# Kernel tuning notes

Measured on AMD Instinct MI355X. Metric: run time of the kernel, lower is better.

The kernel has to match this reference:

```python
import jax, jax.numpy as jnp
import numpy as np

T, N, E = 4, 20000, 320000
F_IN, EH, NH, GH, OUT = 12, 32, 64, 64, 1
NUM_LAYERS = 2
EB_IN = (EH + 2 * NH) * 2 + GH  # 384
NB_IN = 2 * NH + 2 * EH + GH    # 256
GB_IN = NH + EH + GH            # 160


def setup_inputs() -> dict:
    key = jax.random.key(0)
    ks = jax.random.split(key, 24)
    f32 = jnp.float32
    def w(k, fan_in, shape):
        return jax.random.normal(k, shape, f32) * (1.0 / np.sqrt(fan_in))
    return {
        "node_attr": jax.random.normal(ks[0], (T, N, F_IN), f32),
        "edge_attr": jax.random.normal(ks[1], (T, E, 1), f32),
        "edge_index": jax.random.randint(ks[2], (2, E), 0, N, jnp.int32),
        "sp_L_vals": jax.random.normal(ks[3], (E,), f32),
        "global_attr": jax.random.normal(ks[4], (1, GH), f32),
        "coeff": jnp.full((1,), 0.1, f32),
        "W_ee": w(ks[5], 1, (1, EH)), "b_ee": jnp.zeros((EH,), f32),
        "W_ne": w(ks[6], F_IN, (F_IN, NH)), "b_ne": jnp.zeros((NH,), f32),
        "W_eb": w(ks[7], EB_IN, (EB_IN, EH)), "b_eb": jnp.zeros((EH,), f32),
        "W_nb": w(ks[8], NB_IN, (NB_IN, NH)), "b_nb": jnp.zeros((NH,), f32),
        "W_gb": w(ks[9], GB_IN, (GB_IN, GH)), "b_gb": jnp.zeros((GH,), f32),
        "W_nd1": w(ks[10], NH, (NH, NH)), "b_nd1": jnp.zeros((NH,), f32),
        "W_nd2": w(ks[11], NH, (NH, OUT)), "b_nd2": jnp.zeros((OUT,), f32),
    }


def _forward(node_attr, edge_attr, edge_index, sp_L_vals, global_attr, coeff,
             W_ee, b_ee, W_ne, b_ne, W_eb, b_eb, W_nb, b_nb, W_gb, b_gb,
             W_nd1, b_nd1, W_nd2, b_nd2):
    relu = jax.nn.relu
    s, r = edge_index[0], edge_index[1]
    seg = lambda v, idx: jax.ops.segment_sum(v, idx, num_segments=N)
    c = coeff[0]

    # encoders
    x_enc = relu(node_attr @ W_ne + b_ne)   # [T,N,NH]
    e_enc = relu(edge_attr @ W_ee + b_ee)   # [T,E,EH]

    def run_gn(xT, eT, g0):
        # recurrent GN core over processing steps; hidden (h_x,h_e,h_g) starts at zeros
        def step(carry, inp):
            h_x, h_e, h_g = carry
            x_in, e_in = inp
            gE = jnp.broadcast_to(h_g, (E, GH))
            # EdgeBlock: [edge_in, edge_h, sender_in, sender_h, recv_in, recv_h, global]
            edge_cat = jnp.concatenate(
                [e_in, h_e, x_in[s], h_x[s], x_in[r], h_x[r], gE], axis=-1)
            e_new = relu(edge_cat @ W_eb + b_eb)              # [E,EH]
            sent = seg(e_new, s)                              # scatter_add by sender
            recv = seg(e_new, r)                              # scatter_add by receiver
            gN = jnp.broadcast_to(h_g, (N, GH))
            node_cat = jnp.concatenate([x_in, h_x, sent, recv, gN], axis=-1)
            x_new = relu(node_cat @ W_nb + b_nb)              # [N,NH]
            # GlobalBlock: scatter_mean == plain mean (single graph)
            g_cat = jnp.concatenate(
                [x_new.mean(0, keepdims=True), e_new.mean(0, keepdims=True), h_g], axis=-1)
            g_new = relu(g_cat @ W_gb + b_gb)                 # [1,GH]
            # physics terms (pde='diff'): time derivative = state update,
            # spatial derivative = coeff * (graph-Laplacian action via sp_L edge weights)
            t_der = x_new - h_x
            s_der = c * seg(sp_L_vals[:, None] * (x_new[s] - x_new[r]), r)
            return (x_new, e_new, g_new), (x_new, e_new, g_new, t_der, s_der)
        carry0 = (jnp.zeros((N, NH), jnp.float32), jnp.zeros((E, EH), jnp.float32), g0)
        _, ys = jax.lax.scan(step, carry0, (xT, eT))
        return ys  # xs[T,N,NH], es[T,E,EH], gs[T,1,GH], td[T,N,NH], sd[T,N,NH]

    xs, es, gs, td, sd = run_gn(x_enc, e_enc, global_attr)
    x_pre = x_enc
    for _ in range(NUM_LAYERS - 1):
        x_res = xs + x_pre          # residual node state feeds next GN layer
        x_pre = x_res
        xs, es, gs, td, sd = run_gn(x_res, es, gs[0])

    x_final = xs + x_pre            # add_residual=True final residual
    h = relu(x_final @ W_nd1 + b_nd1)
    out_nodes = h @ W_nd2 + b_nd2   # [T,N,OUT]
    return out_nodes, td, sd


def reference(node_attr, edge_attr, edge_index, sp_L_vals, global_attr, coeff,
              W_ee, b_ee, W_ne, b_ne, W_eb, b_eb, W_nb, b_nb, W_gb, b_gb,
              W_nd1, b_nd1, W_nd2, b_nd2):
    return _forward(node_attr, edge_attr, edge_index, sp_L_vals, global_attr, coeff,
                    W_ee, b_ee, W_ne, b_ne, W_eb, b_eb, W_nb, b_nb, W_gb, b_gb,
                    W_nd1, b_nd1, W_nd2, b_nd2)
```

## Files before the change

kernel.cpp:

```cpp
#include <hip/hip_runtime.h>


typedef __attribute__((ext_vector_type(8))) short s16x8;
typedef __attribute__((ext_vector_type(4))) float f32x4;

#define T_STEPS 4
#define NN 20000
#define NP 20224
#define NE 320000

__device__ __forceinline__ float bf2f(unsigned short h){
  return __uint_as_float(((unsigned)h)<<16);
}
__device__ __forceinline__ unsigned short f2bf(float f){
  unsigned u = __float_as_uint(f);
  return (unsigned short)((u + 0x7fffu + ((u>>16)&1u)) >> 16);
}
__device__ __forceinline__ float loadIn(const void* p, size_t i, int bf){
  return bf ? bf2f(((const unsigned short*)p)[i]) : ((const float*)p)[i];
}
__device__ __forceinline__ void storeOut(void* o, size_t i, float v, int bf){
  if(bf) ((unsigned short*)o)[i] = f2bf(v);
  else   ((float*)o)[i] = v;
}
__device__ __forceinline__ void load8(const float* __restrict__ p, float* v){
  const float4* q4 = (const float4*)p;
  float4 a = q4[0], b = q4[1];
  v[0]=a.x; v[1]=a.y; v[2]=a.z; v[3]=a.w;
  v[4]=b.x; v[5]=b.y; v[6]=b.z; v[7]=b.w;
}
__device__ __forceinline__ int4 pack8(const float* v){
  unsigned p0 = (unsigned)f2bf(v[0]) | ((unsigned)f2bf(v[1])<<16);
  unsigned p1 = (unsigned)f2bf(v[2]) | ((unsigned)f2bf(v[3])<<16);
  unsigned p2 = (unsigned)f2bf(v[4]) | ((unsigned)f2bf(v[5])<<16);
  unsigned p3 = (unsigned)f2bf(v[6]) | ((unsigned)f2bf(v[7])<<16);
  return make_int4((int)p0,(int)p1,(int)p2,(int)p3);
}
__device__ __forceinline__ void unp8(int4 w, float* a){
  unsigned x;
  x=(unsigned)w.x; a[0]=__uint_as_float(x<<16); a[1]=__uint_as_float(x&0xffff0000u);
  x=(unsigned)w.y; a[2]=__uint_as_float(x<<16); a[3]=__uint_as_float(x&0xffff0000u);
  x=(unsigned)w.z; a[4]=__uint_as_float(x<<16); a[5]=__uint_as_float(x&0xffff0000u);
  x=(unsigned)w.w; a[6]=__uint_as_float(x<<16); a[7]=__uint_as_float(x&0xffff0000u);
}

union I4S8 { int4 i; s16x8 s; };

__global__ void probe_kernel(const void* coeff_in, int* flagp, float* coeff_f){
  unsigned short u = ((const unsigned short*)coeff_in)[0];
  float as_bf = bf2f(u);
  int f = (fabsf(as_bf - 0.1f) < 0.02f) ? 1 : 0;
  *flagp = f;
  *coeff_f = f ? as_bf : ((const float*)coeff_in)[0];
}

struct ConvJob { const void* src; float* dst; int n; };
struct ConvJobs { ConvJob j[16]; int cnt; };

__global__ void conv_kernel(ConvJobs jobs, const int* flagp, float* z, int zn){
  int bf = *flagp;
  int tid = blockIdx.x*blockDim.x + threadIdx.x;
  int stride = gridDim.x*blockDim.x;
  for(int q=0;q<jobs.cnt;q++){
    const void* s = jobs.j[q].src; float* d = jobs.j[q].dst; int n = jobs.j[q].n;
    for(int i=tid;i<n;i+=stride) d[i] = loadIn(s, i, bf);
  }
  for(int i=tid;i<zn;i+=stride) z[i]=0.f;
}

__global__ void csr_hist(const int* __restrict__ ei, int* deg_s, int* deg_r,
                         unsigned short* __restrict__ rank_s,
                         unsigned short* __restrict__ rank_r){
  int e = blockIdx.x*256+threadIdx.x;
  rank_s[e] = (unsigned short)atomicAdd(&deg_s[ei[e]],1);
  rank_r[e] = (unsigned short)atomicAdd(&deg_r[ei[NE+e]],1);
}

__global__ void csr_scan(const int* __restrict__ deg_s, int* __restrict__ off_s,
                         const int* __restrict__ deg_r, int* __restrict__ off_r){
  const int CH = NP/256;
  const int* deg = blockIdx.x ? deg_r : deg_s;
  int* off = blockIdx.x ? off_r : off_s;
  int t = threadIdx.x;
  int base = t*CH;
  int s = 0;
  #pragma unroll 8
  for(int i=0;i<CH;i++) s += deg[base+i];
  int lane = t & 63, w = t >> 6;
  int x = s;
  #pragma unroll
  for(int o=1;o<64;o<<=1){
    int y = __shfl_up(x, o, 64);
    if(lane >= o) x += y;
  }
  __shared__ int wtot[4];
  if(lane==63) wtot[w] = x;
  __syncthreads();
  int wbase = 0;
  #pragma unroll
  for(int k=0;k<3;k++) if(k<w) wbase += wtot[k];
  int acc = wbase + x - s;
  #pragma unroll 8
  for(int i=0;i<CH;i++){
    off[base+i]=acc; acc+=deg[base+i];
  }
  if(t==255) off[NN]=acc;
}

__global__ void csr_fill(const int* __restrict__ ei,
                         const int* __restrict__ s_off, const int* __restrict__ r_off,
                         const unsigned short* __restrict__ rank_s,
                         const unsigned short* __restrict__ rank_r,
                         int* __restrict__ csr_s, int* __restrict__ csr_r,
                         int2* __restrict__ sr2){
  int e = blockIdx.x*256+threadIdx.x;
  int s = ei[e], r = ei[NE+e];
  sr2[e] = make_int2(s,r);
  csr_s[s_off[s]+rank_s[e]] = e;
  csr_r[r_off[r]+rank_r[e]] = e;
}

__global__ void pack_w_kernel(const void* __restrict__ W,
                              unsigned short* __restrict__ P, int KW, int NT,
                              const int* flagp){
  int bf = *flagp;
  int idx = blockIdx.x*blockDim.x + threadIdx.x;
  int total = NT*KW*512;
  if(idx>=total) return;
  int j = idx & 7;
  int lane = (idx>>3) & 63;
  int rest = idx >> 9;
  int kw = rest % KW;
  int nt = rest / KW;
  int k = kw*32 + (lane>>4)*8 + j;
  int n = nt*16 + (lane&15);
  P[idx] = f2bf(loadIn(W, (size_t)k*(NT*16) + n, bf));
}

__global__ void node_enc_kernel(const void* __restrict__ na,
                                const float* __restrict__ W, const float* __restrict__ b,
                                unsigned short* __restrict__ xA, const int* flagp){
  __shared__ float arow[4][12];
  int bf = *flagp;
  int lane = threadIdx.x & 63, nl = threadIdx.x >> 6;
  int row = blockIdx.x*4 + nl;
  if(lane<12) arow[nl][lane] = loadIn(na, (size_t)row*12+lane, bf);
  __syncthreads();
  float acc = b[lane];
  #pragma unroll
  for(int k=0;k<12;k++) acc += arow[nl][k]*W[k*64+lane];
  xA[(size_t)row*64+lane] = f2bf(fmaxf(acc,0.f));
}

__global__ __launch_bounds__(256) void edge_block_mfma(
  const int2* __restrict__ sr2,
  const unsigned short* __restrict__ x_in,
  const unsigned short* __restrict__ h_x,
  const void* __restrict__ e_attr,
  int e_attr_off,
  const unsigned short* __restrict__ e_in,
  const unsigned short* __restrict__ h_e,
  const float* __restrict__ g,
  const float* __restrict__ W_ee, const float* __restrict__ b_ee,
  const unsigned short* __restrict__ Wp,
  const float* __restrict__ b_eb,
  unsigned short* __restrict__ e_out,
  float* __restrict__ partial_e,
  const int* flagp)
{
  const int tid = threadIdx.x;
  const int lane = tid&63;
  const int q = lane>>4, m16 = lane&15;
  const int pair = blockIdx.x*4 + (tid>>6);
  const int e0 = pair*32;
  const int eg0 = e0 + m16, eg1 = e0 + 16 + m16;
  const int2 sr0 = sr2[eg0], sr1 = sr2[eg1];
  const int o8 = q*8;
  const int4 z4 = make_int4(0,0,0,0);

  I4S8 A0[12], A1[12];
  if(e_attr){
    int bf = *flagp;
    float a0v = loadIn(e_attr, (size_t)e_attr_off + eg0, bf);
    float a1v = loadIn(e_attr, (size_t)e_attr_off + eg1, bf);
    float v[8];
    #pragma unroll
    for(int j=0;j<8;j++) v[j] = fmaxf(a0v*W_ee[o8+j]+b_ee[o8+j], 0.f);
    A0[0].i = pack8(v);
    #pragma unroll
    for(int j=0;j<8;j++) v[j] = fmaxf(a1v*W_ee[o8+j]+b_ee[o8+j], 0.f);
    A1[0].i = pack8(v);
  } else {
    A0[0].i = ((const int4*)(e_in + (size_t)eg0*32))[q];
    A1[0].i = ((const int4*)(e_in + (size_t)eg1*32))[q];
  }
  A0[1].i = h_e ? ((const int4*)(h_e + (size_t)eg0*32))[q] : z4;
  A1[1].i = h_e ? ((const int4*)(h_e + (size_t)eg1*32))[q] : z4;
  { const int4* p0 = (const int4*)(x_in + (size_t)sr0.x*64);
    const int4* p1 = (const int4*)(x_in + (size_t)sr1.x*64);
    A0[2].i = p0[q]; A1[2].i = p1[q];
    A0[3].i = p0[4+q]; A1[3].i = p1[4+q]; }
  if(h_x){
    const int4* p0 = (const int4*)(h_x + (size_t)sr0.x*64);
    const int4* p1 = (const int4*)(h_x + (size_t)sr1.x*64);
    A0[4].i = p0[q]; A1[4].i = p1[q];
    A0[5].i = p0[4+q]; A1[5].i = p1[4+q];
  } else { A0[4].i=z4; A1[4].i=z4; A0[5].i=z4; A1[5].i=z4; }
  { const int4* p0 = (const int4*)(x_in + (size_t)sr0.y*64);
    const int4* p1 = (const int4*)(x_in + (size_t)sr1.y*64);
    A0[6].i = p0[q]; A1[6].i = p1[q];
    A0[7].i = p0[4+q]; A1[7].i = p1[4+q]; }
  if(h_x){
    const int4* p0 = (const int4*)(h_x + (size_t)sr0.y*64);
    const int4* p1 = (const int4*)(h_x + (size_t)sr1.y*64);
    A0[8].i = p0[q]; A1[8].i = p1[q];
    A0[9].i = p0[4+q]; A1[9].i = p1[4+q];
  } else { A0[8].i=z4; A1[8].i=z4; A0[9].i=z4; A1[9].i=z4; }
  { float v[8];
    load8(g + o8, v);      A0[10].i = pack8(v); A1[10].i = A0[10].i;
    load8(g + 32 + o8, v); A0[11].i = pack8(v); A1[11].i = A0[11].i; }

  f32x4 a00={0.f,0.f,0.f,0.f}, a01={0.f,0.f,0.f,0.f};
  f32x4 a10={0.f,0.f,0.f,0.f}, a11={0.f,0.f,0.f,0.f};
  #pragma unroll
  for(int kw=0;kw<12;kw++){
    s16x8 b0 = *(const s16x8*)(Wp + (size_t)(kw*64 + lane)*8);
    s16x8 b1 = *(const s16x8*)(Wp + (size_t)((12+kw)*64 + lane)*8);
    a00 = __builtin_amdgcn_mfma_f32_16x16x32_bf16(A0[kw].s, b0, a00, 0,0,0);
    a01 = __builtin_amdgcn_mfma_f32_16x16x32_bf16(A0[kw].s, b1, a01, 0,0,0);
    a10 = __builtin_amdgcn_mfma_f32_16x16x32_bf16(A1[kw].s, b0, a10, 0,0,0);
    a11 = __builtin_amdgcn_mfma_f32_16x16x32_bf16(A1[kw].s, b1, a11, 0,0,0);
  }

  float pe0=0.f, pe1=0.f;
  const float bb0 = b_eb[m16], bb1 = b_eb[16+m16];
  #pragma unroll
  for(int r=0;r<4;r++){
    int eg0m = e0 + q*4 + r;
    int eg1m = eg0m + 16;
    float v00 = fmaxf(a00[r]+bb0, 0.f);
    float v01 = fmaxf(a01[r]+bb1, 0.f);
    float v10 = fmaxf(a10[r]+bb0, 0.f);
    float v11 = fmaxf(a11[r]+bb1, 0.f);
    e_out[(size_t)eg0m*32+m16]    = f2bf(v00);
    e_out[(size_t)eg0m*32+16+m16] = f2bf(v01);
    e_out[(size_t)eg1m*32+m16]    = f2bf(v10);
    e_out[(size_t)eg1m*32+16+m16] = f2bf(v11);
    pe0 += v00+v10; pe1 += v01+v11;
  }
  pe0 += __shfl_xor(pe0,16,64); pe0 += __shfl_xor(pe0,32,64);
  pe1 += __shfl_xor(pe1,16,64); pe1 += __shfl_xor(pe1,32,64);
  if(q==0){
    int slot = blockIdx.x & 63;
    atomicAdd(&partial_e[slot*32+m16],    pe0);
    atomicAdd(&partial_e[slot*32+16+m16], pe1);
  }
}

__global__ void aggregate_kernel(const unsigned short* __restrict__ e_new,
  const int* __restrict__ s_off, const int* __restrict__ csr_s,
  const int* __restrict__ r_off, const int* __restrict__ csr_r,
  unsigned short* __restrict__ sentB, unsigned short* __restrict__ recvB)
{
  int node = blockIdx.x*4 + (threadIdx.x>>6);
  int lane = threadIdx.x & 63;
  int f = lane & 31, j = lane >> 5;
  float aS0=0.f, aS1=0.f, aR0=0.f, aR1=0.f;
  {
    int beg = s_off[node], end = s_off[node+1];
    int i = beg + j;
    for(; i+2<end; i+=4){
      aS0 += bf2f(e_new[(size_t)csr_s[i]*32 + f]);
      aS1 += bf2f(e_new[(size_t)csr_s[i+2]*32 + f]);
    }
    for(; i<end; i+=2)
      aS0 += bf2f(e_new[(size_t)csr_s[i]*32 + f]);
  }
  {
    int beg = r_off[node], end = r_off[node+1];
    int i = beg + j;
    for(; i+2<end; i+=4){
      aR0 += bf2f(e_new[(size_t)csr_r[i]*32 + f]);
      aR1 += bf2f(e_new[(size_t)csr_r[i+2]*32 + f]);
    }
    for(; i<end; i+=2)
      aR0 += bf2f(e_new[(size_t)csr_r[i]*32 + f]);
  }
  float accS = aS0+aS1, accR = aR0+aR1;
  accS += __shfl_xor(accS,32,64);
  accR += __shfl_xor(accR,32,64);
  if(j==0){
    sentB[(size_t)node*32+f] = f2bf(accS);
    recvB[(size_t)node*32+f] = f2bf(accR);
  }
}

__global__ __launch_bounds__(256) void node_block_mfma(
  const unsigned short* __restrict__ x_in, const unsigned short* __restrict__ h_x,
  const unsigned short* __restrict__ sentB, const unsigned short* __restrict__ recvB,
  const float* __restrict__ g,
  const unsigned short* __restrict__ Wp,
  const float* __restrict__ b_nb,
  unsigned short* __restrict__ x_out, float* __restrict__ partial_x,
  void* __restrict__ out_base, size_t td_off, int has_td,
  const int* flagp)
{
  const int tid = threadIdx.x, lane = tid&63;
  const int q = lane>>4, m16 = lane&15;
  const int tile = blockIdx.x*4 + (tid>>6);
  if(tile >= NN/16) return;
  const int n0 = tile*16;
  const int ng = n0+m16;
  const int o8 = q*8;
  const int4 z4 = make_int4(0,0,0,0);

  I4S8 A[8];
  { const int4* xp = (const int4*)(x_in + (size_t)ng*64);
    A[0].i = xp[q]; A[1].i = xp[4+q]; }
  if(h_x){ const int4* hp = (const int4*)(h_x + (size_t)ng*64);
    A[2].i = hp[q]; A[3].i = hp[4+q];
  } else { A[2].i = z4; A[3].i = z4; }
  A[4].i = ((const int4*)(sentB + (size_t)ng*32))[q];
  A[5].i = ((const int4*)(recvB + (size_t)ng*32))[q];
  { float v[8];
    load8(g + o8, v);      A[6].i = pack8(v);
    load8(g + 32 + o8, v); A[7].i = pack8(v); }

  f32x4 acc[4];
  #pragma unroll
  for(int nt=0;nt<4;nt++) acc[nt] = (f32x4){0.f,0.f,0.f,0.f};
  #pragma unroll
  for(int kw=0;kw<8;kw++){
    #pragma unroll
    for(int nt=0;nt<4;nt++){
      s16x8 b = *(const s16x8*)(Wp + (size_t)((nt*8+kw)*64 + lane)*8);
      acc[nt] = __builtin_amdgcn_mfma_f32_16x16x32_bf16(A[kw].s, b, acc[nt], 0,0,0);
    }
  }

  int bf = has_td ? *flagp : 0;
  float ps[4] = {0.f,0.f,0.f,0.f};
  #pragma unroll
  for(int r=0;r<4;r++){
    int nodeg = n0 + q*4 + r;
    #pragma unroll
    for(int nt=0;nt<4;nt++){
      int col = nt*16 + m16;
      float vv = fmaxf(acc[nt][r] + b_nb[col], 0.f);
      x_out[(size_t)nodeg*64+col] = f2bf(vv);
      if(has_td){
        float hxv = h_x ? bf2f(h_x[(size_t)nodeg*64+col]) : 0.f;
        storeOut(out_base, td_off + (size_t)nodeg*64+col, vv - hxv, bf);
      }
      ps[nt] += vv;
    }
  }
  #pragma unroll
  for(int nt=0;nt<4;nt++){
    ps[nt] += __shfl_xor(ps[nt],16,64);
    ps[nt] += __shfl_xor(ps[nt],32,64);
  }
  if(q==0){
    int slot = blockIdx.x & 63;
    #pragma unroll
    for(int nt=0;nt<4;nt++)
      atomicAdd(&partial_x[slot*64 + nt*16 + m16], ps[nt]);
  }
}

__global__ void global_block_kernel(float* __restrict__ partial_x,
  float* __restrict__ partial_e, const float* __restrict__ h_g,
  const float* __restrict__ W_gb, const float* __restrict__ b_gb,
  float* __restrict__ g_out)
{
  __shared__ float gcat[160];
  __shared__ float red[4][64];
  int tid = threadIdx.x;
  if(tid<64){
    float sx = 0.f;
    #pragma unroll 8
    for(int i=0;i<64;i++) sx += partial_x[i*64+tid];
    gcat[tid] = sx * (1.0f/(float)NN);
  } else if(tid<96){
    int j = tid-64;
    float se = 0.f;
    #pragma unroll 8
    for(int i=0;i<64;i++) se += partial_e[i*32+j];
    gcat[64+j] = se * (1.0f/(float)NE);
  } else if(tid<160){
    gcat[tid] = h_g[tid-96];
  }
  __syncthreads();
  int j = tid&63, c = tid>>6;
  float acc = 0.f;
  #pragma unroll 8
  for(int k=c*40;k<c*40+40;k++) acc += gcat[k]*W_gb[k*64+j];
  red[c][j] = acc;
  __syncthreads();
  for(int i=tid;i<2048;i+=256) partial_e[i]=0.f;
  for(int i=tid;i<4096;i+=256) partial_x[i]=0.f;
  if(tid<64){
    float a = red[0][tid]+red[1][tid]+red[2][tid]+red[3][tid] + b_gb[tid];
    g_out[tid] = fmaxf(a, 0.f);
  }
}

__global__ void sder_csr_kernel(const int2* __restrict__ sr2,
  const void* __restrict__ spL, const unsigned short* __restrict__ x_new,
  const int* __restrict__ r_off, const int* __restrict__ csr_r,
  const float* __restrict__ coeff, void* __restrict__ out_base, size_t off,
  const int* flagp)
{
  int bf = *flagp;
  int lane = threadIdx.x&63, nl = threadIdx.x>>6;
  int node = blockIdx.x*4+nl;
  float xn = bf2f(x_new[(size_t)node*64+lane]);
  float a0=0.f, a1=0.f, a2=0.f, a3=0.f;
  int beg = r_off[node], end = r_off[node+1];
  int i = beg;
  for(; i+4<=end; i+=4){
    int e1 = csr_r[i], e2 = csr_r[i+1], e3 = csr_r[i+2], e4 = csr_r[i+3];
    float w1 = loadIn(spL, e1, bf), w2 = loadIn(spL, e2, bf);
    float w3 = loadIn(spL, e3, bf), w4 = loadIn(spL, e4, bf);
    int s1 = sr2[e1].x, s2 = sr2[e2].x, s3 = sr2[e3].x, s4 = sr2[e4].x;
    a0 += w1*(bf2f(x_new[(size_t)s1*64+lane])-xn);
    a1 += w2*(bf2f(x_new[(size_t)s2*64+lane])-xn);
    a2 += w3*(bf2f(x_new[(size_t)s3*64+lane])-xn);
    a3 += w4*(bf2f(x_new[(size_t)s4*64+lane])-xn);
  }
  for(; i<end; i++){
    int e1 = csr_r[i];
    float w1 = loadIn(spL, e1, bf);
    a0 += w1*(bf2f(x_new[(size_t)sr2[e1].x*64+lane])-xn);
  }
  storeOut(out_base, off + (size_t)node*64+lane, coeff[0]*((a0+a1)+(a2+a3)), bf);
}

__global__ void add_bf16_kernel(const unsigned short* __restrict__ a,
  const unsigned short* __restrict__ b, unsigned short* __restrict__ c, int n){
  int i = blockIdx.x*blockDim.x+threadIdx.x;
  int stride = gridDim.x*blockDim.x;
  for(;i<n;i+=stride) c[i] = f2bf(bf2f(a[i])+bf2f(b[i]));
}

__global__ __launch_bounds__(256) void decoder_kernel(
  const unsigned short* __restrict__ xs, const unsigned short* __restrict__ xr,
  const unsigned short* __restrict__ WpD,
  const float* __restrict__ b1, const float* __restrict__ W2,
  const float* __restrict__ b2,
  void* __restrict__ out_base, const int* flagp)
{
  const int tid=threadIdx.x, lane=tid&63;
  const int q=lane>>4, m16=lane&15;
  const int tile = blockIdx.x*4 + (tid>>6);
  const int row0 = tile*16;
  const int rg = row0 + m16;

  I4S8 A[2];
  #pragma unroll
  for(int kw=0;kw<2;kw++){
    int4 xa = ((const int4*)(xs + (size_t)rg*64 + kw*32))[q];
    int4 xb = ((const int4*)(xr + (size_t)rg*64 + kw*32))[q];
    float va[8], vb[8], v[8];
    unp8(xa, va); unp8(xb, vb);
    #pragma unroll
    for(int j=0;j<8;j++) v[j] = va[j]+vb[j];
    A[kw].i = pack8(v);
  }

  f32x4 acc[4];
  #pragma unroll
  for(int nt=0;nt<4;nt++) acc[nt] = (f32x4){0.f,0.f,0.f,0.f};
  #pragma unroll
  for(int kw=0;kw<2;kw++){
    #pragma unroll
    for(int nt=0;nt<4;nt++){
      s16x8 b = *(const s16x8*)(WpD + (size_t)((nt*2+kw)*64 + lane)*8);
      acc[nt] = __builtin_amdgcn_mfma_f32_16x16x32_bf16(A[kw].s, b, acc[nt], 0,0,0);
    }
  }

  float val[4];
  #pragma unroll
  for(int r=0;r<4;r++){
    float s = 0.f;
    #pragma unroll
    for(int nt=0;nt<4;nt++){
      int col = nt*16 + m16;
      s += fmaxf(acc[nt][r] + b1[col], 0.f) * W2[col];
    }
    val[r] = s;
  }
  #pragma unroll
  for(int o=1;o<16;o<<=1){
    #pragma unroll
    for(int r=0;r<4;r++) val[r] += __shfl_xor(val[r], o, 64);
  }
  if(m16==0){
    int bf = *flagp;
    float bb = b2[0];
    #pragma unroll
    for(int r=0;r<4;r++)
      storeOut(out_base, (size_t)(row0 + q*4 + r), val[r] + bb, bf);
  }
}

extern "C" void kernel_launch(void* const* d_in, const int* in_sizes, int n_in,
                              void* d_out, int out_size, void* d_ws, size_t ws_size,
                              hipStream_t stream){
  const void* node_attr = d_in[0];
  const void* edge_attr = d_in[1];
  const int*  ei        = (const int*)d_in[2];
  const void* spL       = d_in[3];
  const void* gattr     = d_in[4];
  const void* coeff_in  = d_in[5];
  const void* W_ee_in = d_in[6];  const void* b_ee_in = d_in[7];
  const void* W_ne_in = d_in[8];  const void* b_ne_in = d_in[9];
  const void* W_eb_in = d_in[10]; const void* b_eb_in = d_in[11];
  const void* W_nb_in = d_in[12]; const void* b_nb_in = d_in[13];
  const void* W_gb_in = d_in[14]; const void* b_gb_in = d_in[15];
  const void* W_nd1_in= d_in[16]; const void* b_nd1_in= d_in[17];
  const void* W_nd2_in= d_in[18]; const void* b_nd2_in= d_in[19];

  float* ws = (float*)d_ws;
  float* W_ee_f = ws;             float* b_ee_f = W_ee_f+32;
  float* W_ne_f = b_ee_f+32;      float* b_ne_f = W_ne_f+768;
  float* W_gb_f = b_ne_f+64;      float* b_gb_f = W_gb_f+10240;
  float* W_nd1_f= b_gb_f+64;      float* b_nd1_f= W_nd1_f+4096;
  float* W_nd2_f= b_nd1_f+64;     float* b_nd2_f= W_nd2_f+64;
  float* b_eb_f = b_nd2_f+1;      float* b_nb_f = b_eb_f+32;
  float* coeff_f= b_nb_f+64;
  int*   flagp  = (int*)(ws + 15523);
  float* gbuf   = ws + 15524;
  float* part_e = ws + 16100;
  float* part_x = part_e + 2048;
  int*   deg_s  = (int*)(part_x + 4096);
  int*   deg_r  = deg_s + NP;
  int*   s_off  = deg_r + NP;
  int*   r_off  = s_off + NP+1;
  unsigned short* rank_s = (unsigned short*)(r_off + NP+1);
  unsigned short* rank_r = rank_s + NE;
  int*   csr_s  = (int*)(rank_r + NE);
  int*   csr_r  = csr_s + NE;
  size_t iend   = (size_t)((int*)(csr_r + NE) - (int*)ws);
  iend = (iend + 3) & ~(size_t)3;
  int2*  sr2    = (int2*)(ws + iend);
  unsigned short* sentB = (unsigned short*)(sr2 + NE);
  unsigned short* recvB = sentB + (size_t)NN*32;
  unsigned short* eBuf  = recvB + (size_t)NN*32;
  unsigned short* xA    = eBuf + (size_t)T_STEPS*NE*32;
  unsigned short* xB    = xA + (size_t)T_STEPS*NN*64;
  unsigned short* xC    = xB + (size_t)T_STEPS*NN*64;
  unsigned short* WpE   = xC + (size_t)T_STEPS*NN*64;
  unsigned short* WpN   = WpE + 12288;
  unsigned short* WpD   = WpN + 16384;

  probe_kernel<<<1,1,0,stream>>>(coeff_in, flagp, coeff_f);

  ConvJobs jobs; int c=0;
  auto add=[&](const void* s, float* d, int n){ jobs.j[c].src=s; jobs.j[c].dst=d; jobs.j[c].n=n; c++; };
  add(W_ee_in,W_ee_f,32);   add(b_ee_in,b_ee_f,32);
  add(W_ne_in,W_ne_f,768);  add(b_ne_in,b_ne_f,64);
  add(W_gb_in,W_gb_f,10240);add(b_gb_in,b_gb_f,64);
  add(W_nd1_in,W_nd1_f,4096);add(b_nd1_in,b_nd1_f,64);
  add(W_nd2_in,W_nd2_f,64); add(b_nd2_in,b_nd2_f,1);
  add(b_eb_in,b_eb_f,32);   add(b_nb_in,b_nb_f,64);
  add(gattr,gbuf,64);
  jobs.cnt=c;
  conv_kernel<<<64,256,0,stream>>>(jobs, flagp, part_e, 2048+4096+2*NP);

  csr_hist<<<NE/256,256,0,stream>>>(ei, deg_s, deg_r, rank_s, rank_r);
  csr_scan<<<2,256,0,stream>>>(deg_s, s_off, deg_r, r_off);
  csr_fill<<<NE/256,256,0,stream>>>(ei, s_off, r_off, rank_s, rank_r, csr_s, csr_r, sr2);

  pack_w_kernel<<<48,256,0,stream>>>(W_eb_in, WpE, 12, 2, flagp);
  pack_w_kernel<<<64,256,0,stream>>>(W_nb_in, WpN, 8, 4, flagp);
  pack_w_kernel<<<16,256,0,stream>>>(W_nd1_in, WpD, 2, 4, flagp);

  node_enc_kernel<<<T_STEPS*NN/4,256,0,stream>>>(node_attr, W_ne_f, b_ne_f, xA, flagp);

  const size_t td_base = (size_t)T_STEPS*NN;
  const size_t sd_base = td_base + (size_t)T_STEPS*NN*64;

  for(int layer=0; layer<2; layer++){
    for(int t=0;t<T_STEPS;t++){
      const unsigned short* x_in = (layer==0? xA : xC) + (size_t)t*NN*64;
      const unsigned short* h_x  = (t>0)? xB + (size_t)(t-1)*NN*64 : nullptr;
      const unsigned short* h_e  = (t>0)? eBuf + (size_t)(t-1)*NE*32 : nullptr;
      const float* gptr = (layer==0)? gbuf + t*64
                                    : (t==0? gbuf+1*64 : gbuf+(4+t)*64);
      float*       gout = (layer==0)? gbuf+(1+t)*64 : gbuf+(5+t)*64;
      const void*  eat  = (layer==0)? edge_attr : nullptr;
      const unsigned short* e_in = (layer==0)? nullptr : eBuf + (size_t)t*NE*32;
      unsigned short*       e_out= eBuf + (size_t)t*NE*32;

      edge_block_mfma<<<NE/128,256,0,stream>>>(sr2, x_in, h_x, eat, t*NE, e_in, h_e, gptr,
          W_ee_f, b_ee_f, WpE, b_eb_f, e_out, part_e, flagp);

      aggregate_kernel<<<NN/4,256,0,stream>>>(e_out, s_off, csr_s, r_off, csr_r,
          sentB, recvB);

      unsigned short* x_out = xB + (size_t)t*NN*64;
      size_t td_off = td_base + (size_t)t*NN*64;
      node_block_mfma<<<(NN/16+3)/4,256,0,stream>>>(x_in, h_x, sentB, recvB, gptr,
          WpN, b_nb_f, x_out, part_x, d_out, td_off, (layer==1)?1:0, flagp);

      global_block_kernel<<<1,256,0,stream>>>(part_x, part_e, gptr, W_gb_f, b_gb_f, gout);

      if(layer==1){
        sder_csr_kernel<<<NN/4,256,0,stream>>>(sr2, spL, x_out, r_off, csr_r,
            coeff_f, d_out, sd_base + (size_t)t*NN*64, flagp);
      }
    }
    if(layer==0){
      add_bf16_kernel<<<2048,256,0,stream>>>(xA, xB, xC, T_STEPS*NN*64);
    }
  }

  decoder_kernel<<<(T_STEPS*NN/16+3)/4,256,0,stream>>>(xB, xC, WpD,
      b_nd1_f, W_nd2_f, b_nd2_f, d_out, flagp);
}
```

Measured before the change: 940.7 us.

## Store edges in receiver-sorted order to make receiver aggregation contiguous

```diff
diff --git a/kernel.cpp b/kernel.cpp
--- a/kernel.cpp
+++ b/kernel.cpp
@@ -112,12 +112,16 @@
                          const unsigned short* __restrict__ rank_s,
                          const unsigned short* __restrict__ rank_r,
                          int* __restrict__ csr_s, int* __restrict__ csr_r,
-                         int2* __restrict__ sr2){
+                         int2* __restrict__ sr2,
+                         const void* __restrict__ spL, float* __restrict__ spL_p,
+                         const int* flagp){
   int e = blockIdx.x*256+threadIdx.x;
   int s = ei[e], r = ei[NE+e];
-  sr2[e] = make_int2(s,r);
-  csr_s[s_off[s]+rank_s[e]] = e;
-  csr_r[r_off[r]+rank_r[e]] = e;
+  int p = r_off[r] + rank_r[e];
+  sr2[p] = make_int2(s,r);
+  csr_r[p] = e;
+  csr_s[s_off[s]+rank_s[e]] = p;
+  spL_p[p] = loadIn(spL, e, *flagp);
 }
 
 __global__ void pack_w_kernel(const void* __restrict__ W,
@@ -158,6 +162,7 @@
   const unsigned short* __restrict__ h_x,
   const void* __restrict__ e_attr,
   int e_attr_off,
+  const int* __restrict__ inv,
   const unsigned short* __restrict__ e_in,
   const unsigned short* __restrict__ h_e,
   const float* __restrict__ g,
@@ -181,8 +186,8 @@
   I4S8 A0[12], A1[12];
   if(e_attr){
     int bf = *flagp;
-    float a0v = loadIn(e_attr, (size_t)e_attr_off + eg0, bf);
-    float a1v = loadIn(e_attr, (size_t)e_attr_off + eg1, bf);
+    float a0v = loadIn(e_attr, (size_t)e_attr_off + inv[eg0], bf);
+    float a1v = loadIn(e_attr, (size_t)e_attr_off + inv[eg1], bf);
     float v[8];
     #pragma unroll
     for(int j=0;j<8;j++) v[j] = fmaxf(a0v*W_ee[o8+j]+b_ee[o8+j], 0.f);
@@ -259,7 +264,7 @@
 
 __global__ void aggregate_kernel(const unsigned short* __restrict__ e_new,
   const int* __restrict__ s_off, const int* __restrict__ csr_s,
-  const int* __restrict__ r_off, const int* __restrict__ csr_r,
+  const int* __restrict__ r_off,
   unsigned short* __restrict__ sentB, unsigned short* __restrict__ recvB)
 {
   int node = blockIdx.x*4 + (threadIdx.x>>6);
@@ -280,11 +285,11 @@
     int beg = r_off[node], end = r_off[node+1];
     int i = beg + j;
     for(; i+2<end; i+=4){
-      aR0 += bf2f(e_new[(size_t)csr_r[i]*32 + f]);
-      aR1 += bf2f(e_new[(size_t)csr_r[i+2]*32 + f]);
+      aR0 += bf2f(e_new[(size_t)i*32 + f]);
+      aR1 += bf2f(e_new[(size_t)(i+2)*32 + f]);
     }
     for(; i<end; i+=2)
-      aR0 += bf2f(e_new[(size_t)csr_r[i]*32 + f]);
+      aR0 += bf2f(e_new[(size_t)i*32 + f]);
   }
   float accS = aS0+aS1, accR = aR0+aR1;
   accS += __shfl_xor(accS,32,64);
@@ -406,8 +411,8 @@
 }
 
 __global__ void sder_csr_kernel(const int2* __restrict__ sr2,
-  const void* __restrict__ spL, const unsigned short* __restrict__ x_new,
-  const int* __restrict__ r_off, const int* __restrict__ csr_r,
+  const float* __restrict__ spL_p, const unsigned short* __restrict__ x_new,
+  const int* __restrict__ r_off,
   const float* __restrict__ coeff, void* __restrict__ out_base, size_t off,
   const int* flagp)
 {
@@ -419,19 +424,17 @@
   int beg = r_off[node], end = r_off[node+1];
   int i = beg;
   for(; i+4<=end; i+=4){
-    int e1 = csr_r[i], e2 = csr_r[i+1], e3 = csr_r[i+2], e4 = csr_r[i+3];
-    float w1 = loadIn(spL, e1, bf), w2 = loadIn(spL, e2, bf);
-    float w3 = loadIn(spL, e3, bf), w4 = loadIn(spL, e4, bf);
-    int s1 = sr2[e1].x, s2 = sr2[e2].x, s3 = sr2[e3].x, s4 = sr2[e4].x;
+    float w1 = spL_p[i],   w2 = spL_p[i+1];
+    float w3 = spL_p[i+2], w4 = spL_p[i+3];
+    int s1 = sr2[i].x, s2 = sr2[i+1].x, s3 = sr2[i+2].x, s4 = sr2[i+3].x;
     a0 += w1*(bf2f(x_new[(size_t)s1*64+lane])-xn);
     a1 += w2*(bf2f(x_new[(size_t)s2*64+lane])-xn);
     a2 += w3*(bf2f(x_new[(size_t)s3*64+lane])-xn);
     a3 += w4*(bf2f(x_new[(size_t)s4*64+lane])-xn);
   }
   for(; i<end; i++){
-    int e1 = csr_r[i];
-    float w1 = loadIn(spL, e1, bf);
-    a0 += w1*(bf2f(x_new[(size_t)sr2[e1].x*64+lane])-xn);
+    float w1 = spL_p[i];
+    a0 += w1*(bf2f(x_new[(size_t)sr2[i].x*64+lane])-xn);
   }
   storeOut(out_base, off + (size_t)node*64+lane, coeff[0]*((a0+a1)+(a2+a3)), bf);
 }
@@ -542,7 +545,8 @@
   unsigned short* rank_r = rank_s + NE;
   int*   csr_s  = (int*)(rank_r + NE);
   int*   csr_r  = csr_s + NE;
-  size_t iend   = (size_t)((int*)(csr_r + NE) - (int*)ws);
+  float* spL_p  = (float*)(csr_r + NE);
+  size_t iend   = (size_t)((int*)(spL_p + NE) - (int*)ws);
   iend = (iend + 3) & ~(size_t)3;
   int2*  sr2    = (int2*)(ws + iend);
   unsigned short* sentB = (unsigned short*)(sr2 + NE);
@@ -571,7 +575,8 @@
 
   csr_hist<<<NE/256,256,0,stream>>>(ei, deg_s, deg_r, rank_s, rank_r);
   csr_scan<<<2,256,0,stream>>>(deg_s, s_off, deg_r, r_off);
-  csr_fill<<<NE/256,256,0,stream>>>(ei, s_off, r_off, rank_s, rank_r, csr_s, csr_r, sr2);
+  csr_fill<<<NE/256,256,0,stream>>>(ei, s_off, r_off, rank_s, rank_r,
+      csr_s, csr_r, sr2, spL, spL_p, flagp);
 
   pack_w_kernel<<<48,256,0,stream>>>(W_eb_in, WpE, 12, 2, flagp);
   pack_w_kernel<<<64,256,0,stream>>>(W_nb_in, WpN, 8, 4, flagp);
@@ -594,10 +599,10 @@
       const unsigned short* e_in = (layer==0)? nullptr : eBuf + (size_t)t*NE*32;
       unsigned short*       e_out= eBuf + (size_t)t*NE*32;
 
-      edge_block_mfma<<<NE/128,256,0,stream>>>(sr2, x_in, h_x, eat, t*NE, e_in, h_e, gptr,
-          W_ee_f, b_ee_f, WpE, b_eb_f, e_out, part_e, flagp);
-
-      aggregate_kernel<<<NN/4,256,0,stream>>>(e_out, s_off, csr_s, r_off, csr_r,
+      edge_block_mfma<<<NE/128,256,0,stream>>>(sr2, x_in, h_x, eat, t*NE, csr_r,
+          e_in, h_e, gptr, W_ee_f, b_ee_f, WpE, b_eb_f, e_out, part_e, flagp);
+
+      aggregate_kernel<<<NN/4,256,0,stream>>>(e_out, s_off, csr_s, r_off,
           sentB, recvB);
 
       unsigned short* x_out = xB + (size_t)t*NN*64;
@@ -608,7 +613,7 @@
       global_block_kernel<<<1,256,0,stream>>>(part_x, part_e, gptr, W_gb_f, b_gb_f, gout);
 
       if(layer==1){
-        sder_csr_kernel<<<NN/4,256,0,stream>>>(sr2, spL, x_out, r_off, csr_r,
+        sder_csr_kernel<<<NN/4,256,0,stream>>>(sr2, spL_p, x_out, r_off,
             coeff_f, d_out, sd_base + (size_t)t*NN*64, flagp);
       }
     }
```

After: 845.7 us. -10.1%, faster.
